# Performance work log

Hardware: AMD Instinct MI355X
Metric: run time of the kernel (lower is better)

The kernel has to match this reference:

```python
import jax, jax.numpy as jnp
import numpy as np

N_NODES = 20000
N_EDGES = 320000
DIMS = [256, 256, 128, 64]  # input_dim, hidden_dims...
EPS = 1e-5


def gcn_conv(x, w, b, src, dst, n):
    # PyG GCNConv: linear first, then symmetric-normalized aggregation with self-loops
    x = x @ w  # [N, out]
    loops = jnp.arange(n, dtype=src.dtype)
    src2 = jnp.concatenate([src, loops])
    dst2 = jnp.concatenate([dst, loops])
    deg = jax.ops.segment_sum(jnp.ones_like(dst2, dtype=x.dtype), dst2, num_segments=n)
    dinv = jnp.where(deg > 0, deg ** -0.5, 0.0)
    norm = dinv[src2] * dinv[dst2]  # [E+N]
    msg = x[src2] * norm[:, None]   # gathered, scaled messages
    out = jax.ops.segment_sum(msg, dst2, num_segments=n)
    return out + b


def graph_norm(x, w, b, a):
    # PyG GraphNorm over a single graph: per-feature mean/var across nodes
    mean = jnp.mean(x, axis=0)
    centered = x - a * mean
    var = jnp.mean(centered * centered, axis=0)
    return w * centered * jax.lax.rsqrt(var + EPS) + b


def layer_norm(x, w, b):
    mean = jnp.mean(x, axis=-1, keepdims=True)
    var = jnp.mean((x - mean) ** 2, axis=-1, keepdims=True)
    return (x - mean) * jax.lax.rsqrt(var + EPS) * w + b


def setup_inputs() -> dict:
    key = jax.random.key(0)
    ks = jax.random.split(key, 32)
    inp = {}
    inp["x"] = jax.random.normal(ks[0], (N_NODES, DIMS[0]), dtype=jnp.float32)
    inp["edge_index"] = jax.random.randint(ks[1], (2, N_EDGES), 0, N_NODES, dtype=jnp.int32)
    ki = 2
    for i in range(3):
        fin, fout = DIMS[i], DIMS[i + 1]
        s = 1.0 / np.sqrt(fin)
        inp[f"w{i}"] = jax.random.uniform(ks[ki], (fin, fout), jnp.float32, -s, s); ki += 1
        inp[f"b{i}"] = jnp.zeros((fout,), jnp.float32)
        inp[f"gn{i}_w"] = jnp.ones((fout,), jnp.float32)
        inp[f"gn{i}_b"] = jnp.zeros((fout,), jnp.float32)
        inp[f"gn{i}_a"] = jnp.ones((fout,), jnp.float32)
    h = DIMS[-1]
    s = 1.0 / np.sqrt(3 * h)
    inp["wc1"] = jax.random.uniform(ks[ki], (3 * h, h), jnp.float32, -s, s); ki += 1
    inp["bc1"] = jnp.zeros((h,), jnp.float32)
    inp["ln_w"] = jnp.ones((h,), jnp.float32)
    inp["ln_b"] = jnp.zeros((h,), jnp.float32)
    s = 1.0 / np.sqrt(h)
    inp["wc2"] = jax.random.uniform(ks[ki], (h, 2), jnp.float32, -s, s); ki += 1
    inp["bc2"] = jnp.zeros((2,), jnp.float32)
    return inp


def reference(x, edge_index,
              w0, b0, gn0_w, gn0_b, gn0_a,
              w1, b1, gn1_w, gn1_b, gn1_a,
              w2, b2, gn2_w, gn2_b, gn2_a,
              wc1, bc1, ln_w, ln_b, wc2, bc2):
    src, dst = edge_index[0], edge_index[1]
    n = x.shape[0]
    params = [(w0, b0, gn0_w, gn0_b, gn0_a),
              (w1, b1, gn1_w, gn1_b, gn1_a),
              (w2, b2, gn2_w, gn2_b, gn2_a)]
    for (w, b, gw, gb, ga) in params:
        x_res = x
        x = gcn_conv(x, w, b, src, dst, n)
        x = graph_norm(x, gw, gb, ga)
        x = jax.nn.gelu(x, approximate=False)
        # dropout = identity (eval); residual only when shapes match (layer 0)
        if x.shape == x_res.shape:
            x = x + x_res
    # multi-pool over the single graph (batch vector of zeros): mean | max | sum
    pooled = jnp.concatenate([jnp.mean(x, axis=0), jnp.max(x, axis=0), jnp.sum(x, axis=0)])[None, :]  # [1, 3h]
    h = pooled @ wc1 + bc1
    h = layer_norm(h, ln_w, ln_b)
    h = jax.nn.gelu(h, approximate=False)
    return h @ wc2 + bc2  # [1, num_classes]
```

## Files before the change

kernel.cpp:

```cpp
#include <hip/hip_runtime.h>
#include <math.h>

#define EPSV 1e-5f
#define MAXB 2176
#define GBLK 2080

typedef __attribute__((ext_vector_type(8))) short short8;
typedef __attribute__((ext_vector_type(4))) float f32x4;

__device__ __forceinline__ float gelu_f(float x) {
    return 0.5f * x * (1.0f + erff(x * 0.70710678118654752440f));
}

__device__ __forceinline__ float4 f4add(float4 a, float4 b) {
    return make_float4(a.x + b.x, a.y + b.y, a.z + b.z, a.w + b.w);
}

__device__ __forceinline__ ushort f2bf(float v) {
    union { float f; unsigned u; } a; a.f = v;
    unsigned r = a.u + 0x7FFFu + ((a.u >> 16) & 1u);
    return (ushort)(r >> 16);
}
__device__ __forceinline__ float bf2f(ushort h) {
    union { unsigned u; float f; } a; a.u = ((unsigned)h) << 16;
    return a.f;
}

__global__ void deg_kernel(const int* __restrict__ ei, int* __restrict__ deg, int E) {
    int stride = gridDim.x * blockDim.x;
    for (int e = blockIdx.x * blockDim.x + threadIdx.x; e < E; e += stride)
        atomicAdd(&deg[ei[E + e]], 1);
}

__global__ void dinv_kernel(const int* __restrict__ deg, float* __restrict__ dinv, int N) {
    int i = blockIdx.x * blockDim.x + threadIdx.x;
    if (i < N) dinv[i] = rsqrtf((float)(deg[i] + 1));
}

__global__ __launch_bounds__(1024) void scan_kernel(const int* __restrict__ deg,
                                                    int* __restrict__ off, int N) {
    __shared__ int sh[1024];
    int t = threadIdx.x;
    int chunk = (N + 1023) >> 10;
    int b = t * chunk;
    int e = b + chunk; if (e > N) e = N;
    int s = 0;
    for (int i = b; i < e; ++i) s += deg[i];
    sh[t] = s;
    __syncthreads();
    for (int d = 1; d < 1024; d <<= 1) {
        int v = (t >= d) ? sh[t - d] : 0;
        __syncthreads();
        sh[t] += v;
        __syncthreads();
    }
    int run = (t > 0) ? sh[t - 1] : 0;
    for (int i = b; i < e; ++i) { off[i] = run; run += deg[i]; }
    if (t == 1023) off[N] = sh[1023];
}

__global__ void fill_kernel(const int* __restrict__ ei, const int* __restrict__ off,
                            int* __restrict__ fill, int* __restrict__ csr, int E) {
    int stride = gridDim.x * blockDim.x;
    for (int e = blockIdx.x * blockDim.x + threadIdx.x; e < E; e += stride) {
        int d = ei[E + e];
        int p = off[d] + atomicAdd(&fill[d], 1);
        csr[p] = ei[e];
    }
}

__global__ __launch_bounds__(256) void packx_kernel(
    const float* __restrict__ x, ushort* __restrict__ hi, ushort* __restrict__ lo, long n)
{
    long stride = (long)gridDim.x * blockDim.x * 4;
    for (long i = ((long)blockIdx.x * blockDim.x + threadIdx.x) * 4; i < n; i += stride) {
        float4 v = *(const float4*)(x + i);
        ushort4 h, l2;
        h.x = f2bf(v.x); h.y = f2bf(v.y); h.z = f2bf(v.z); h.w = f2bf(v.w);
        l2.x = f2bf(v.x - bf2f(h.x)); l2.y = f2bf(v.y - bf2f(h.y));
        l2.z = f2bf(v.z - bf2f(h.z)); l2.w = f2bf(v.w - bf2f(h.w));
        *(ushort4*)(hi + i) = h;
        *(ushort4*)(lo + i) = l2;
    }
}

__global__ void packw_kernel(const float* __restrict__ W, ushort* __restrict__ wthi,
                             ushort* __restrict__ wtlo, int K, int F)
{
    int idx = blockIdx.x * 256 + threadIdx.x;
    if (idx >= K * F) return;
    int k = idx / F, f = idx - k * F;
    float v = W[idx];
    ushort h = f2bf(v);
    wthi[f * K + k] = h;
    wtlo[f * K + k] = f2bf(v - bf2f(h));
}

template<int K, int BN>
__global__ __launch_bounds__(256) void gemm_mfma_kernel(
    const ushort* __restrict__ ahi, const ushort* __restrict__ alo,
    const ushort* __restrict__ wthi, const ushort* __restrict__ wtlo,
    const float* __restrict__ dinv, float* __restrict__ C,
    int M, int F)
{
    constexpr int BM = 128, BK = 64;
    constexpr int LDK = BK + 8;
    constexpr int CF  = BN / 32;
    constexpr int WCH = BN / 32;

    __shared__ ushort AsH[BM * LDK], AsL[BM * LDK];
    __shared__ ushort WsH[BN * LDK], WsL[BN * LDK];

    const int tid = threadIdx.x;
    const int l = tid & 63, w = tid >> 6;
    const int wr = w >> 1, wc = w & 1;
    const int m0   = blockIdx.y * BM;
    const int colB = blockIdx.x * BN;
    const int lr = l & 15, lkg = l >> 4;

    f32x4 acc[4][CF] = {};

    for (int kk = 0; kk < K; kk += BK) {
        short8 ra[4], rb[4], rwh[WCH], rwl[WCH];
#pragma unroll
        for (int i = 0; i < 4; ++i) {
            int q = tid + i * 256;
            int row = q >> 3, cc = q & 7;
            int rg = m0 + row; if (rg > M - 1) rg = M - 1;
            ra[i] = *(const short8*)(ahi + (size_t)rg * K + kk + cc * 8);
            rb[i] = *(const short8*)(alo + (size_t)rg * K + kk + cc * 8);
        }
#pragma unroll
        for (int i = 0; i < WCH; ++i) {
            int q = tid + i * 256;
            int row = q >> 3, cc = q & 7;
            rwh[i] = *(const short8*)(wthi + (size_t)(colB + row) * K + kk + cc * 8);
            rwl[i] = *(const short8*)(wtlo + (size_t)(colB + row) * K + kk + cc * 8);
        }
        __syncthreads();
#pragma unroll
        for (int i = 0; i < 4; ++i) {
            int q = tid + i * 256;
            int row = q >> 3, cc = q & 7;
            *(short8*)&AsH[row * LDK + cc * 8] = ra[i];
            *(short8*)&AsL[row * LDK + cc * 8] = rb[i];
        }
#pragma unroll
        for (int i = 0; i < WCH; ++i) {
            int q = tid + i * 256;
            int row = q >> 3, cc = q & 7;
            *(short8*)&WsH[row * LDK + cc * 8] = rwh[i];
            *(short8*)&WsL[row * LDK + cc * 8] = rwl[i];
        }
        __syncthreads();

#pragma unroll
        for (int ks = 0; ks < 2; ++ks) {
            const int kof = ks * 32 + lkg * 8;
            short8 afh[4], afl[4];
#pragma unroll
            for (int rf = 0; rf < 4; ++rf) {
                int row = wr * 64 + rf * 16 + lr;
                afh[rf] = *(const short8*)&AsH[row * LDK + kof];
                afl[rf] = *(const short8*)&AsL[row * LDK + kof];
            }
            short8 wfh[CF], wfl[CF];
#pragma unroll
            for (int cf = 0; cf < CF; ++cf) {
                int row = wc * (BN / 2) + cf * 16 + lr;
                wfh[cf] = *(const short8*)&WsH[row * LDK + kof];
                wfl[cf] = *(const short8*)&WsL[row * LDK + kof];
            }
#pragma unroll
            for (int rf = 0; rf < 4; ++rf) {
#pragma unroll
                for (int cf = 0; cf < CF; ++cf) {
                    acc[rf][cf] = __builtin_amdgcn_mfma_f32_16x16x32_bf16(afh[rf], wfh[cf], acc[rf][cf], 0, 0, 0);
                    acc[rf][cf] = __builtin_amdgcn_mfma_f32_16x16x32_bf16(afh[rf], wfl[cf], acc[rf][cf], 0, 0, 0);
                    acc[rf][cf] = __builtin_amdgcn_mfma_f32_16x16x32_bf16(afl[rf], wfh[cf], acc[rf][cf], 0, 0, 0);
                }
            }
        }
    }

#pragma unroll
    for (int rf = 0; rf < 4; ++rf) {
#pragma unroll
        for (int j = 0; j < 4; ++j) {
            int r = m0 + wr * 64 + rf * 16 + lkg * 4 + j;
            if (r < M) {
                float dv = dinv[r];
                float* Cp = C + (size_t)r * F + colB + wc * (BN / 2) + lr;
#pragma unroll
                for (int cf = 0; cf < CF; ++cf)
                    Cp[cf * 16] = acc[rf][cf][j] * dv;
            }
        }
    }
}

template<int F>
__global__ __launch_bounds__(256) void gather_kernel(
    const float* __restrict__ hs, const int* __restrict__ off,
    const int* __restrict__ csr, const float* __restrict__ dinv,
    const float* __restrict__ bias, float* __restrict__ t,
    float* __restrict__ p1, float* __restrict__ p2, int N)
{
    constexpr int NG  = F / 64;
    constexpr int LDR = F / 4;
    constexpr int NPB = 16;
    const int lane = threadIdx.x & 15;
    const int slot = threadIdx.x >> 4;

    const int xs    = blockIdx.x & 7;
    const int g     = xs % NG;
    const int r     = xs / NG;
    const int chunk = blockIdx.x >> 3;
    const int repl  = 8 / NG;
    const int nPerG = (int)(gridDim.x >> 3) * repl;
    const int j     = chunk * repl + r;

    const int col4 = g * 16 + lane;
    const float4* hs4 = (const float4*)hs;
    float4* t4 = (float4*)t;
    const float4 bv = ((const float4*)bias)[col4];

    float4 a1 = make_float4(0.f, 0.f, 0.f, 0.f);
    float4 a2 = make_float4(0.f, 0.f, 0.f, 0.f);

    for (int d = j * NPB + slot; d < N; d += nPerG * NPB) {
        float4 acc = hs4[(long)d * LDR + col4];
        const int e0 = off[d], e1 = off[d + 1];
        int e = e0;
        for (; e + 8 <= e1; e += 8) {
            int s0 = csr[e + 0], s1 = csr[e + 1], s2 = csr[e + 2], s3 = csr[e + 3];
            int s4 = csr[e + 4], s5 = csr[e + 5], s6 = csr[e + 6], s7 = csr[e + 7];
            float4 v0 = hs4[(long)s0 * LDR + col4];
            float4 v1 = hs4[(long)s1 * LDR + col4];
            float4 v2 = hs4[(long)s2 * LDR + col4];
            float4 v3 = hs4[(long)s3 * LDR + col4];
            float4 v4 = hs4[(long)s4 * LDR + col4];
            float4 v5 = hs4[(long)s5 * LDR + col4];
            float4 v6 = hs4[(long)s6 * LDR + col4];
            float4 v7 = hs4[(long)s7 * LDR + col4];
            float4 u0 = f4add(v0, v1);
            float4 u1 = f4add(v2, v3);
            float4 u2 = f4add(v4, v5);
            float4 u3 = f4add(v6, v7);
            acc = f4add(acc, f4add(f4add(u0, u1), f4add(u2, u3)));
        }
        for (; e + 2 <= e1; e += 2) {
            int s0 = csr[e + 0], s1 = csr[e + 1];
            acc = f4add(acc, f4add(hs4[(long)s0 * LDR + col4], hs4[(long)s1 * LDR + col4]));
        }
        if (e < e1) {
            acc = f4add(acc, hs4[(long)csr[e] * LDR + col4]);
        }

        float dv = dinv[d];
        float4 o;
        o.x = fmaf(dv, acc.x, bv.x);
        o.y = fmaf(dv, acc.y, bv.y);
        o.z = fmaf(dv, acc.z, bv.z);
        o.w = fmaf(dv, acc.w, bv.w);
        t4[(long)d * LDR + col4] = o;
        a1.x += o.x; a1.y += o.y; a1.z += o.z; a1.w += o.w;
        a2.x += o.x * o.x; a2.y += o.y * o.y; a2.z += o.z * o.z; a2.w += o.w * o.w;
    }

    __shared__ float red[8][256];
    red[0][threadIdx.x] = a1.x; red[1][threadIdx.x] = a1.y;
    red[2][threadIdx.x] = a1.z; red[3][threadIdx.x] = a1.w;
    red[4][threadIdx.x] = a2.x; red[5][threadIdx.x] = a2.y;
    red[6][threadIdx.x] = a2.z; red[7][threadIdx.x] = a2.w;
    __syncthreads();
    if (slot == 0) {
        float sum[8];
#pragma unroll
        for (int k = 0; k < 8; ++k) {
            float s = red[k][lane];
            for (int jj = 1; jj < NPB; ++jj) s += red[k][jj * 16 + lane];
            sum[k] = s;
        }
        ((float4*)p1)[(long)col4 * MAXB + blockIdx.x] = make_float4(sum[0], sum[1], sum[2], sum[3]);
        ((float4*)p2)[(long)col4 * MAXB + blockIdx.x] = make_float4(sum[4], sum[5], sum[6], sum[7]);
    }
}

__global__ __launch_bounds__(256) void statreduce_kernel(
    const float* __restrict__ p1, const float* __restrict__ p2,
    const float* __restrict__ ga,
    float* __restrict__ meanv, float* __restrict__ istdv,
    int nb, int N, int NG)
{
    const int c4 = blockIdx.x;
    const int g = (c4 >> 4) % NG;
    const float4* p14 = (const float4*)p1 + (long)c4 * MAXB;
    const float4* p24 = (const float4*)p2 + (long)c4 * MAXB;
    float4 a1 = make_float4(0.f, 0.f, 0.f, 0.f);
    float4 a2 = make_float4(0.f, 0.f, 0.f, 0.f);
    for (int r = threadIdx.x; r < nb; r += 256) {
        if (((r & 7) % NG) != g) continue;
        float4 v1 = p14[r];
        float4 v2 = p24[r];
        a1.x += v1.x; a1.y += v1.y; a1.z += v1.z; a1.w += v1.w;
        a2.x += v2.x; a2.y += v2.y; a2.z += v2.z; a2.w += v2.w;
    }
#pragma unroll
    for (int offv = 32; offv > 0; offv >>= 1) {
        a1.x += __shfl_down(a1.x, offv); a1.y += __shfl_down(a1.y, offv);
        a1.z += __shfl_down(a1.z, offv); a1.w += __shfl_down(a1.w, offv);
        a2.x += __shfl_down(a2.x, offv); a2.y += __shfl_down(a2.y, offv);
        a2.z += __shfl_down(a2.z, offv); a2.w += __shfl_down(a2.w, offv);
    }
    __shared__ float4 sh1[4], sh2[4];
    const int wid = threadIdx.x >> 6;
    if ((threadIdx.x & 63) == 0) { sh1[wid] = a1; sh2[wid] = a2; }
    __syncthreads();
    if (threadIdx.x == 0) {
        float4 t1 = sh1[0], t2 = sh2[0];
        for (int jj = 1; jj < 4; ++jj) {
            float4 u1 = sh1[jj], u2 = sh2[jj];
            t1.x += u1.x; t1.y += u1.y; t1.z += u1.z; t1.w += u1.w;
            t2.x += u2.x; t2.y += u2.y; t2.z += u2.z; t2.w += u2.w;
        }
        float s1a[4] = { t1.x, t1.y, t1.z, t1.w };
        float s2a[4] = { t2.x, t2.y, t2.z, t2.w };
#pragma unroll
        for (int k = 0; k < 4; ++k) {
            int c = c4 * 4 + k;
            float m = s1a[k] / (float)N;
            float a = ga[c];
            float var = s2a[k] / (float)N - 2.f * a * m * m + a * a * m * m;
            meanv[c] = m;
            istdv[c] = rsqrtf(var + EPSV);
        }
    }
}

__global__ __launch_bounds__(256) void normgelu_kernel(
    const float* __restrict__ t, const float* __restrict__ meanv,
    const float* __restrict__ istdv, const float* __restrict__ gw,
    const float* __restrict__ gb, const float* __restrict__ ga,
    const float* __restrict__ res,
    ushort* __restrict__ ohi, ushort* __restrict__ olo,
    float* __restrict__ fpout,
    int log2f, long total)
{
    long stride = (long)gridDim.x * blockDim.x;
    int fmask = (1 << log2f) - 1;
    for (long idx = (long)blockIdx.x * blockDim.x + threadIdx.x; idx < total; idx += stride) {
        int c = (int)idx & fmask;
        float v = t[idx];
        float y = gw[c] * (v - ga[c] * meanv[c]) * istdv[c] + gb[c];
        y = gelu_f(y);
        if (res) y += res[idx];
        if (ohi) {
            ushort h = f2bf(y);
            ohi[idx] = h;
            olo[idx] = f2bf(y - bf2f(h));
        } else {
            fpout[idx] = y;
        }
    }
}

__device__ __forceinline__ void atomicMaxFloat(float* addr, float val) {
    unsigned* ua = (unsigned*)addr;
    unsigned old = *ua;
    while (true) {
        float of = __uint_as_float(old);
        if (of >= val) break;
        unsigned assumed = old;
        old = atomicCAS(ua, assumed, __float_as_uint(val));
        if (old == assumed) break;
    }
}

__global__ void initpool_kernel(float* __restrict__ psum, float* __restrict__ pmax) {
    int t = threadIdx.x;
    psum[t] = 0.f;
    pmax[t] = -INFINITY;
}

__global__ __launch_bounds__(256) void colpool_kernel(
    const float* __restrict__ x, float* __restrict__ psum, float* __restrict__ pmax,
    int M, int rowsPerBlock)
{
    int c = threadIdx.x & 63;
    int rl = threadIdx.x >> 6;
    int r0 = blockIdx.x * rowsPerBlock;
    int rend = r0 + rowsPerBlock; if (rend > M) rend = M;
    float a1 = 0.f, am = -INFINITY;
    for (int r = r0 + rl; r < rend; r += 4) {
        float v = x[(long)r * 64 + c];
        a1 += v; am = fmaxf(am, v);
    }
    __shared__ float sh1[256], shm[256];
    sh1[threadIdx.x] = a1; shm[threadIdx.x] = am;
    __syncthreads();
    if (threadIdx.x < 64) {
        for (int j = 1; j < 4; ++j) {
            a1 += sh1[c + j * 64];
            am = fmaxf(am, shm[c + j * 64]);
        }
        atomicAdd(&psum[c], a1);
        atomicMaxFloat(&pmax[c], am);
    }
}

__global__ void head_kernel(const float* __restrict__ psum, const float* __restrict__ pmax,
                            const float* __restrict__ wc1, const float* __restrict__ bc1,
                            const float* __restrict__ lnw, const float* __restrict__ lnb,
                            const float* __restrict__ wc2, const float* __restrict__ bc2,
                            float* __restrict__ out, int M)
{
    __shared__ float p[192];
    int t = threadIdx.x;
    float s = psum[t];
    p[t] = s / (float)M;
    p[64 + t] = pmax[t];
    p[128 + t] = s;
    __syncthreads();
    float h = bc1[t];
    for (int k = 0; k < 192; ++k) h = fmaf(p[k], wc1[k * 64 + t], h);
    float m = h;
    for (int off = 32; off > 0; off >>= 1) m += __shfl_xor(m, off);
    m *= (1.f / 64.f);
    float d = h - m;
    float v = d * d;
    for (int off = 32; off > 0; off >>= 1) v += __shfl_xor(v, off);
    v *= (1.f / 64.f);
    float y = d * rsqrtf(v + EPSV) * lnw[t] + lnb[t];
    y = gelu_f(y);
    float o0 = y * wc2[t * 2 + 0];
    float o1 = y * wc2[t * 2 + 1];
    for (int off = 32; off > 0; off >>= 1) {
        o0 += __shfl_xor(o0, off);
        o1 += __shfl_xor(o1, off);
    }
    if (t == 0) {
        out[0] = o0 + bc2[0];
        out[1] = o1 + bc2[1];
    }
}

extern "C" void kernel_launch(void* const* d_in, const int* in_sizes, int n_in,
                              void* d_out, int out_size, void* d_ws, size_t ws_size,
                              hipStream_t stream)
{
    const float* x    = (const float*)d_in[0];
    const int*   ei   = (const int*)d_in[1];
    const float* w0   = (const float*)d_in[2];
    const float* b0   = (const float*)d_in[3];
    const float* gn0w = (const float*)d_in[4];
    const float* gn0b = (const float*)d_in[5];
    const float* gn0a = (const float*)d_in[6];
    const float* w1   = (const float*)d_in[7];
    const float* b1   = (const float*)d_in[8];
    const float* gn1w = (const float*)d_in[9];
    const float* gn1b = (const float*)d_in[10];
    const float* gn1a = (const float*)d_in[11];
    const float* w2   = (const float*)d_in[12];
    const float* b2   = (const float*)d_in[13];
    const float* gn2w = (const float*)d_in[14];
    const float* gn2b = (const float*)d_in[15];
    const float* gn2a = (const float*)d_in[16];
    const float* wc1  = (const float*)d_in[17];
    const float* bc1  = (const float*)d_in[18];
    const float* lnw  = (const float*)d_in[19];
    const float* lnb  = (const float*)d_in[20];
    const float* wc2  = (const float*)d_in[21];
    const float* bc2  = (const float*)d_in[22];

    const int N = in_sizes[0] / 256;
    const int E = in_sizes[1] / 2;

    float* ws = (float*)d_ws;
    const size_t BIG = (size_t)N * 256;
    float* B0    = ws;
    float* B1    = ws + BIG;
    float* dinv  = ws + 2 * BIG;
    int*   deg   = (int*)(dinv + N);
    int*   off   = deg + N;
    int*   fill  = off + N + 1;
    int*   csr   = fill + N;
    float* p1    = (float*)(csr + E);
    float* p2    = p1 + (size_t)64 * MAXB * 4;
    float* meanv = p2 + (size_t)64 * MAXB * 4;
    float* istdv = meanv + 256;
    float* psum  = istdv + 256;
    float* pmax  = psum + 64;
    ushort* wthi = (ushort*)(pmax + 64);
    ushort* wtlo = wthi + 256 * 256;

    hipMemsetAsync(deg, 0, (size_t)N * sizeof(int), stream);
    hipMemsetAsync(fill, 0, (size_t)N * sizeof(int), stream);
    deg_kernel<<<1024, 256, 0, stream>>>(ei, deg, E);
    dinv_kernel<<<(N + 255) / 256, 256, 0, stream>>>(deg, dinv, N);
    scan_kernel<<<1, 1024, 0, stream>>>(deg, off, N);
    fill_kernel<<<1024, 256, 0, stream>>>(ei, off, fill, csr, E);

    packx_kernel<<<1280, 256, 0, stream>>>(x, (ushort*)B0, (ushort*)B0 + BIG, (long)BIG);

    struct Layer {
        const float *w, *b, *gw, *gb, *ga;
        int K, F, lf;
    } L[3] = {
        { w0, b0, gn0w, gn0b, gn0a, 256, 256, 8 },
        { w1, b1, gn1w, gn1b, gn1a, 256, 128, 7 },
        { w2, b2, gn2w, gn2b, gn2a, 128,  64, 6 },
    };
    const float* resb[3] = { x, nullptr, nullptr };
    float* Bb[2] = { B0, B1 };

    int cur = 0;
    for (int li = 0; li < 3; ++li) {
        const int K = L[li].K, F = L[li].F, lf = L[li].lf;
        const long total = (long)N << lf;
        float* Ab = Bb[cur];
        float* HS = Bb[cur ^ 1];
        ushort* ahi = (ushort*)Ab;
        ushort* alo = ahi + BIG;

        packw_kernel<<<(K * F + 255) / 256, 256, 0, stream>>>(L[li].w, wthi, wtlo, K, F);

        const int rowTiles = (N + 127) / 128;
        if (li == 0) {
            gemm_mfma_kernel<256, 128><<<dim3(2, rowTiles), 256, 0, stream>>>(
                ahi, alo, wthi, wtlo, dinv, HS, N, F);
        } else if (li == 1) {
            gemm_mfma_kernel<256, 128><<<dim3(1, rowTiles), 256, 0, stream>>>(
                ahi, alo, wthi, wtlo, dinv, HS, N, F);
        } else {
            gemm_mfma_kernel<128, 64><<<dim3(1, rowTiles), 256, 0, stream>>>(
                ahi, alo, wthi, wtlo, dinv, HS, N, F);
        }

        float* T = Ab;
        if (F == 256)
            gather_kernel<256><<<GBLK, 256, 0, stream>>>(HS, off, csr, dinv, L[li].b, T, p1, p2, N);
        else if (F == 128)
            gather_kernel<128><<<GBLK, 256, 0, stream>>>(HS, off, csr, dinv, L[li].b, T, p1, p2, N);
        else
            gather_kernel<64><<<GBLK, 256, 0, stream>>>(HS, off, csr, dinv, L[li].b, T, p1, p2, N);

        statreduce_kernel<<<F / 4, 256, 0, stream>>>(p1, p2, L[li].ga, meanv, istdv, GBLK, N, F / 64);

        long fb = (total + 255) / 256; if (fb > 4096) fb = 4096;
        ushort* ohi = (li < 2) ? (ushort*)HS : nullptr;
        ushort* olo = (li < 2) ? (ushort*)HS + BIG : nullptr;
        float*  fpo = (li == 2) ? HS : nullptr;
        normgelu_kernel<<<(int)fb, 256, 0, stream>>>(T, meanv, istdv,
                                                     L[li].gw, L[li].gb, L[li].ga,
                                                     resb[li], ohi, olo, fpo, lf, total);
        cur ^= 1;
    }

    initpool_kernel<<<1, 64, 0, stream>>>(psum, pmax);
    colpool_kernel<<<(N + 127) / 128, 256, 0, stream>>>(Bb[cur], psum, pmax, N, 128);
    head_kernel<<<1, 64, 0, stream>>>(psum, pmax, wc1, bc1, lnw, lnb, wc2, bc2,
                                      (float*)d_out, N);
}
```

Before: 294.7 us.

## Store GEMM output as bf16 for gather, fuse dinv and weight packing launches

```diff
diff --git a/kernel.cpp b/kernel.cpp
--- a/kernel.cpp
+++ b/kernel.cpp
@@ -25,6 +25,9 @@
     union { unsigned u; float f; } a; a.u = ((unsigned)h) << 16;
     return a.f;
 }
+__device__ __forceinline__ float4 bf4f(ushort4 v) {
+    return make_float4(bf2f(v.x), bf2f(v.y), bf2f(v.z), bf2f(v.w));
+}
 
 __global__ void deg_kernel(const int* __restrict__ ei, int* __restrict__ deg, int E) {
     int stride = gridDim.x * blockDim.x;
@@ -32,13 +35,9 @@
         atomicAdd(&deg[ei[E + e]], 1);
 }
 
-__global__ void dinv_kernel(const int* __restrict__ deg, float* __restrict__ dinv, int N) {
-    int i = blockIdx.x * blockDim.x + threadIdx.x;
-    if (i < N) dinv[i] = rsqrtf((float)(deg[i] + 1));
-}
-
 __global__ __launch_bounds__(1024) void scan_kernel(const int* __restrict__ deg,
-                                                    int* __restrict__ off, int N) {
+                                                    int* __restrict__ off,
+                                                    float* __restrict__ dinv, int N) {
     __shared__ int sh[1024];
     int t = threadIdx.x;
     int chunk = (N + 1023) >> 10;
@@ -55,7 +54,11 @@
         __syncthreads();
     }
     int run = (t > 0) ? sh[t - 1] : 0;
-    for (int i = b; i < e; ++i) { off[i] = run; run += deg[i]; }
+    for (int i = b; i < e; ++i) {
+        off[i] = run;
+        run += deg[i];
+        dinv[i] = rsqrtf((float)(deg[i] + 1));
+    }
     if (t == 1023) off[N] = sh[1023];
 }
 
@@ -84,23 +87,28 @@
     }
 }
 
-__global__ void packw_kernel(const float* __restrict__ W, ushort* __restrict__ wthi,
-                             ushort* __restrict__ wtlo, int K, int F)
+__global__ void packw_all_kernel(const float* __restrict__ w0, const float* __restrict__ w1,
+                                 const float* __restrict__ w2,
+                                 ushort* __restrict__ wthi, ushort* __restrict__ wtlo)
 {
     int idx = blockIdx.x * 256 + threadIdx.x;
-    if (idx >= K * F) return;
-    int k = idx / F, f = idx - k * F;
-    float v = W[idx];
+    const float* W; int K, F, base, local;
+    if (idx < 65536)       { W = w0; K = 256; F = 256; base = 0;     local = idx; }
+    else if (idx < 98304)  { W = w1; K = 256; F = 128; base = 65536; local = idx - 65536; }
+    else if (idx < 106496) { W = w2; K = 128; F = 64;  base = 98304; local = idx - 98304; }
+    else return;
+    int k = local / F, f = local - k * F;
+    float v = W[local];
     ushort h = f2bf(v);
-    wthi[f * K + k] = h;
-    wtlo[f * K + k] = f2bf(v - bf2f(h));
+    wthi[base + f * K + k] = h;
+    wtlo[base + f * K + k] = f2bf(v - bf2f(h));
 }
 
 template<int K, int BN>
 __global__ __launch_bounds__(256) void gemm_mfma_kernel(
     const ushort* __restrict__ ahi, const ushort* __restrict__ alo,
     const ushort* __restrict__ wthi, const ushort* __restrict__ wtlo,
-    const float* __restrict__ dinv, float* __restrict__ C,
+    const float* __restrict__ dinv, ushort* __restrict__ C,
     int M, int F)
 {
     constexpr int BM = 128, BK = 64;
@@ -190,10 +198,10 @@
             int r = m0 + wr * 64 + rf * 16 + lkg * 4 + j;
             if (r < M) {
                 float dv = dinv[r];
-                float* Cp = C + (size_t)r * F + colB + wc * (BN / 2) + lr;
+                ushort* Cp = C + (size_t)r * F + colB + wc * (BN / 2) + lr;
 #pragma unroll
                 for (int cf = 0; cf < CF; ++cf)
-                    Cp[cf * 16] = acc[rf][cf][j] * dv;
+                    Cp[cf * 16] = f2bf(acc[rf][cf][j] * dv);
             }
         }
     }
@@ -201,7 +209,7 @@
 
 template<int F>
 __global__ __launch_bounds__(256) void gather_kernel(
-    const float* __restrict__ hs, const int* __restrict__ off,
+    const ushort* __restrict__ hs, const int* __restrict__ off,
     const int* __restrict__ csr, const float* __restrict__ dinv,
     const float* __restrict__ bias, float* __restrict__ t,
     float* __restrict__ p1, float* __restrict__ p2, int N)
@@ -221,7 +229,7 @@
     const int j     = chunk * repl + r;
 
     const int col4 = g * 16 + lane;
-    const float4* hs4 = (const float4*)hs;
+    const int c0 = col4 * 4;
     float4* t4 = (float4*)t;
     const float4 bv = ((const float4*)bias)[col4];
 
@@ -229,32 +237,34 @@
     float4 a2 = make_float4(0.f, 0.f, 0.f, 0.f);
 
     for (int d = j * NPB + slot; d < N; d += nPerG * NPB) {
-        float4 acc = hs4[(long)d * LDR + col4];
+        float4 acc = bf4f(*(const ushort4*)(hs + (size_t)d * F + c0));
         const int e0 = off[d], e1 = off[d + 1];
         int e = e0;
         for (; e + 8 <= e1; e += 8) {
             int s0 = csr[e + 0], s1 = csr[e + 1], s2 = csr[e + 2], s3 = csr[e + 3];
             int s4 = csr[e + 4], s5 = csr[e + 5], s6 = csr[e + 6], s7 = csr[e + 7];
-            float4 v0 = hs4[(long)s0 * LDR + col4];
-            float4 v1 = hs4[(long)s1 * LDR + col4];
-            float4 v2 = hs4[(long)s2 * LDR + col4];
-            float4 v3 = hs4[(long)s3 * LDR + col4];
-            float4 v4 = hs4[(long)s4 * LDR + col4];
-            float4 v5 = hs4[(long)s5 * LDR + col4];
-            float4 v6 = hs4[(long)s6 * LDR + col4];
-            float4 v7 = hs4[(long)s7 * LDR + col4];
-            float4 u0 = f4add(v0, v1);
-            float4 u1 = f4add(v2, v3);
-            float4 u2 = f4add(v4, v5);
-            float4 u3 = f4add(v6, v7);
+            ushort4 v0 = *(const ushort4*)(hs + (size_t)s0 * F + c0);
+            ushort4 v1 = *(const ushort4*)(hs + (size_t)s1 * F + c0);
+            ushort4 v2 = *(const ushort4*)(hs + (size_t)s2 * F + c0);
+            ushort4 v3 = *(const ushort4*)(hs + (size_t)s3 * F + c0);
+            ushort4 v4 = *(const ushort4*)(hs + (size_t)s4 * F + c0);
+            ushort4 v5 = *(const ushort4*)(hs + (size_t)s5 * F + c0);
+            ushort4 v6 = *(const ushort4*)(hs + (size_t)s6 * F + c0);
+            ushort4 v7 = *(const ushort4*)(hs + (size_t)s7 * F + c0);
+            float4 u0 = f4add(bf4f(v0), bf4f(v1));
+            float4 u1 = f4add(bf4f(v2), bf4f(v3));
+            float4 u2 = f4add(bf4f(v4), bf4f(v5));
+            float4 u3 = f4add(bf4f(v6), bf4f(v7));
             acc = f4add(acc, f4add(f4add(u0, u1), f4add(u2, u3)));
         }
         for (; e + 2 <= e1; e += 2) {
             int s0 = csr[e + 0], s1 = csr[e + 1];
-            acc = f4add(acc, f4add(hs4[(long)s0 * LDR + col4], hs4[(long)s1 * LDR + col4]));
+            ushort4 v0 = *(const ushort4*)(hs + (size_t)s0 * F + c0);
+            ushort4 v1 = *(const ushort4*)(hs + (size_t)s1 * F + c0);
+            acc = f4add(acc, f4add(bf4f(v0), bf4f(v1)));
         }
         if (e < e1) {
-            acc = f4add(acc, hs4[(long)csr[e] * LDR + col4]);
+            acc = f4add(acc, bf4f(*(const ushort4*)(hs + (size_t)csr[e] * F + c0)));
         }
 
         float dv = dinv[d];
@@ -482,9 +492,9 @@
     float* B1    = ws + BIG;
     float* dinv  = ws + 2 * BIG;
     int*   deg   = (int*)(dinv + N);
-    int*   off   = deg + N;
-    int*   fill  = off + N + 1;
-    int*   csr   = fill + N;
+    int*   fill  = deg + N;
+    int*   off   = fill + N;
+    int*   csr   = off + N + 1;
     float* p1    = (float*)(csr + E);
     float* p2    = p1 + (size_t)64 * MAXB * 4;
     float* meanv = p2 + (size_t)64 * MAXB * 4;
@@ -492,24 +502,24 @@
     float* psum  = istdv + 256;
     float* pmax  = psum + 64;
     ushort* wthi = (ushort*)(pmax + 64);
-    ushort* wtlo = wthi + 256 * 256;
-
-    hipMemsetAsync(deg, 0, (size_t)N * sizeof(int), stream);
-    hipMemsetAsync(fill, 0, (size_t)N * sizeof(int), stream);
+    ushort* wtlo = wthi + 106496;
+    const int woff[3] = { 0, 65536, 98304 };
+
+    hipMemsetAsync(deg, 0, (size_t)2 * N * sizeof(int), stream);
     deg_kernel<<<1024, 256, 0, stream>>>(ei, deg, E);
-    dinv_kernel<<<(N + 255) / 256, 256, 0, stream>>>(deg, dinv, N);
-    scan_kernel<<<1, 1024, 0, stream>>>(deg, off, N);
+    scan_kernel<<<1, 1024, 0, stream>>>(deg, off, dinv, N);
     fill_kernel<<<1024, 256, 0, stream>>>(ei, off, fill, csr, E);
 
+    packw_all_kernel<<<416, 256, 0, stream>>>(w0, w1, w2, wthi, wtlo);
     packx_kernel<<<1280, 256, 0, stream>>>(x, (ushort*)B0, (ushort*)B0 + BIG, (long)BIG);
 
     struct Layer {
-        const float *w, *b, *gw, *gb, *ga;
+        const float *b, *gw, *gb, *ga;
         int K, F, lf;
     } L[3] = {
-        { w0, b0, gn0w, gn0b, gn0a, 256, 256, 8 },
-        { w1, b1, gn1w, gn1b, gn1a, 256, 128, 7 },
-        { w2, b2, gn2w, gn2b, gn2a, 128,  64, 6 },
+        { b0, gn0w, gn0b, gn0a, 256, 256, 8 },
+        { b1, gn1w, gn1b, gn1a, 256, 128, 7 },
+        { b2, gn2w, gn2b, gn2a, 128,  64, 6 },
     };
     const float* resb[3] = { x, nullptr, nullptr };
     float* Bb[2] = { B0, B1 };
@@ -519,22 +529,21 @@
         const int K = L[li].K, F = L[li].F, lf = L[li].lf;
         const long total = (long)N << lf;
         float* Ab = Bb[cur];
-        float* HS = Bb[cur ^ 1];
+        float* HSf = Bb[cur ^ 1];
         ushort* ahi = (ushort*)Ab;
         ushort* alo = ahi + BIG;
-
-        packw_kernel<<<(K * F + 255) / 256, 256, 0, stream>>>(L[li].w, wthi, wtlo, K, F);
+        ushort* HS = (ushort*)HSf;
 
         const int rowTiles = (N + 127) / 128;
         if (li == 0) {
             gemm_mfma_kernel<256, 128><<<dim3(2, rowTiles), 256, 0, stream>>>(
-                ahi, alo, wthi, wtlo, dinv, HS, N, F);
+                ahi, alo, wthi + woff[0], wtlo + woff[0], dinv, HS, N, F);
         } else if (li == 1) {
             gemm_mfma_kernel<256, 128><<<dim3(1, rowTiles), 256, 0, stream>>>(
-                ahi, alo, wthi, wtlo, dinv, HS, N, F);
+                ahi, alo, wthi + woff[1], wtlo + woff[1], dinv, HS, N, F);
         } else {
             gemm_mfma_kernel<128, 64><<<dim3(1, rowTiles), 256, 0, stream>>>(
-                ahi, alo, wthi, wtlo, dinv, HS, N, F);
+                ahi, alo, wthi + woff[2], wtlo + woff[2], dinv, HS, N, F);
         }
 
         float* T = Ab;
@@ -548,9 +557,9 @@
         statreduce_kernel<<<F / 4, 256, 0, stream>>>(p1, p2, L[li].ga, meanv, istdv, GBLK, N, F / 64);
 
         long fb = (total + 255) / 256; if (fb > 4096) fb = 4096;
-        ushort* ohi = (li < 2) ? (ushort*)HS : nullptr;
-        ushort* olo = (li < 2) ? (ushort*)HS + BIG : nullptr;
-        float*  fpo = (li == 2) ? HS : nullptr;
+        ushort* ohi = (li < 2) ? (ushort*)HSf : nullptr;
+        ushort* olo = (li < 2) ? (ushort*)HSf + BIG : nullptr;
+        float*  fpo = (li == 2) ? HSf : nullptr;
         normgelu_kernel<<<(int)fb, 256, 0, stream>>>(T, meanv, istdv,
                                                      L[li].gw, L[li].gb, L[li].ga,
                                                      resb[li], ohi, olo, fpo, lf, total);
```

Result: faster. 280.0 us (-5.0%).
